# Performance work log

Hardware: AMD Instinct MI355X
Metric: run time of the kernel (lower is better)

## Reference

```python
import jax, jax.numpy as jnp
import numpy as np

# ---- config ----
N = 500000
C = 32            # output_coordinate_dim
RES = [256, 256, 256, 64]
J = 2             # wavelet levels
BOUNDS = 1.3
# plane i -> (H, W) of stored plane, and (q, r) coord indices into [x,y,z,t]
# grid_sample convention: coord0 indexes W, coord1 indexes H
PLANE_RES = [(256, 256), (256, 256), (256, 64), (256, 256), (256, 64), (256, 64)]
COORD_IDX = [(0, 1), (0, 2), (3, 0), (1, 2), (3, 1), (3, 2)]

# coif4 decomposition low-pass filter (pywt), 24 taps
DEC_LO = np.array([
    -1.7849850030882614e-06, -3.2596802368833675e-06, 3.1229875865345646e-05,
    6.233903446100713e-05, -0.00025997455248771324, -0.0005890207562443383,
    0.0012665619292989445, 0.003751436157278457, -0.00565828668661072,
    -0.015211731527946259, 0.025082261844864097, 0.03933442712333749,
    -0.09622044203398798, -0.06662747426342504, 0.4343860564914685,
    0.782238930920499, 0.41530840703043026, -0.05607731331675481,
    -0.08126669968087875, 0.026682300156053072, 0.016068943964776348,
    -0.0073461663276420935, -0.0016294920126017326, 0.0008923136685823146],
    dtype=np.float32)
REC_LO = DEC_LO[::-1].copy()                                    # synthesis low-pass
REC_HI = (DEC_LO * ((-1.0) ** np.arange(DEC_LO.shape[0]))).astype(np.float32)  # QMF high-pass


def _up2(x, axis):
    """Insert zeros between samples along axis (upsample by 2)."""
    x = jnp.moveaxis(x, axis, -1)
    z = jnp.zeros(x.shape[:-1] + (2 * x.shape[-1],), x.dtype)
    z = z.at[..., ::2].set(x)
    return jnp.moveaxis(z, -1, axis)


def _circ_conv(x, f, axis):
    """Circular convolution along axis with a short fixed filter (periodization mode)."""
    out = f[0] * x
    for k in range(1, len(f)):
        out = out + f[k] * jnp.roll(x, k, axis=axis)
    return out


def _sfb1d(lo, hi, axis):
    """1D synthesis filter bank: upsample, filter, add. Length L -> 2L."""
    return _circ_conv(_up2(lo, axis), REC_LO, axis) + _circ_conv(_up2(hi, axis), REC_HI, axis)


def _sfb_level(ll, yh):
    """One inverse-DWT level. ll: [1,C,h,w], yh: [1,C,3,h,w] -> [1,C,2h,2w]."""
    lh, hl, hh = yh[:, :, 0], yh[:, :, 1], yh[:, :, 2]
    lo = _sfb1d(ll, lh, axis=2)   # combine along H
    hi = _sfb1d(hl, hh, axis=2)
    return _sfb1d(lo, hi, axis=3)  # combine along W


def _idwt2(yl, yhb, yha):
    """2-level inverse DWT (coif4, periodization). yl coarsest, yhb coarse detail, yha fine detail."""
    x = _sfb_level(yl, yhb)   # H/4 -> H/2
    x = _sfb_level(x, yha)    # H/2 -> H
    return x                  # [1, C, H, W]


def _bilinear_sample(plane, coords):
    """torch.grid_sample(bilinear, align_corners=True) equivalent.
    plane: [C,H,W]; coords: [N,2] in [-1,1], coords[:,0]->W, coords[:,1]->H. Returns [N,C]."""
    Cc, H, W = plane.shape
    x = jnp.clip((coords[:, 0] + 1.0) * 0.5 * (W - 1), 0.0, W - 1.0)
    y = jnp.clip((coords[:, 1] + 1.0) * 0.5 * (H - 1), 0.0, H - 1.0)
    x0 = jnp.clip(jnp.floor(x), 0.0, W - 2.0)
    y0 = jnp.clip(jnp.floor(y), 0.0, H - 2.0)
    wx = x - x0
    wy = y - y0
    x0i = x0.astype(jnp.int32); x1i = x0i + 1
    y0i = y0.astype(jnp.int32); y1i = y0i + 1
    v = (plane[:, y0i, x0i] * (1 - wy) * (1 - wx)
         + plane[:, y0i, x1i] * (1 - wy) * wx
         + plane[:, y1i, x0i] * wy * (1 - wx)
         + plane[:, y1i, x1i] * wy * wx)  # [C,N]
    return v.T


def setup_inputs() -> dict:
    key = jax.random.key(0)
    keys = jax.random.split(key, 2 + 6 * 3)
    inp = {}
    inp["pts"] = jax.random.uniform(keys[0], (N, 3), jnp.float32, -BOUNDS, BOUNDS)
    inp["timestamps"] = jax.random.uniform(keys[1], (N, 1), jnp.float32, 0.0, 1.0)
    for i, (H, W) in enumerate(PLANE_RES):
        k0, k1, k2 = keys[2 + 3 * i], keys[2 + 3 * i + 1], keys[2 + 3 * i + 2]
        # wavelet-domain learned parameters: yl coarsest approx, yha fine detail, yhb coarse detail
        inp[f"yl{i}"] = 0.3 + 0.1 * jax.random.normal(k0, (1, C, H // 4, W // 4), jnp.float32)
        inp[f"yha{i}"] = 0.05 * jax.random.normal(k1, (1, C, 3, H // 2, W // 2), jnp.float32)
        inp[f"yhb{i}"] = 0.05 * jax.random.normal(k2, (1, C, 3, H // 4, W // 4), jnp.float32)
    return inp


def reference(pts, timestamps,
              yl0, yha0, yhb0, yl1, yha1, yhb1, yl2, yha2, yhb2,
              yl3, yha3, yhb3, yl4, yha4, yhb4, yl5, yha5, yhb5):
    coefs = [(yl0, yha0, yhb0), (yl1, yha1, yhb1), (yl2, yha2, yhb2),
             (yl3, yha3, yhb3), (yl4, yha4, yhb4), (yl5, yha5, yhb5)]
    # normalize_aabb with aabb = [[B,B,B],[-B,-B,-B]]
    pts_n = (pts - BOUNDS) * (2.0 / (-2.0 * BOUNDS)) - 1.0
    t = timestamps * 2.0 - 1.0
    p4 = jnp.concatenate([pts_n, t], axis=-1)  # [N,4] = (x,y,z,t) in [-1,1]
    interp = jnp.ones((), jnp.float32)
    for (yl, yha, yhb), (q, r) in zip(coefs, COORD_IDX):
        plane = _idwt2(yl, yhb, yha)[0]                      # [C,H,W] IDWT reconstruction
        coords = jnp.stack([p4[:, q], p4[:, r]], axis=-1)    # [N,2]
        feat = _bilinear_sample(plane, coords)               # [N,C] gather
        interp = interp * feat                               # multiplicative fusion
    return interp
```

## Files before the change

### kernel.cpp

```cpp
#include <hip/hip_runtime.h>
#include <hip/hip_fp16.h>

#define NBIN 4096
#define NREP 8
#define SCAP 32
#define OVCAP 65536

__device__ __constant__ float DEC_LO[24] = {
    -1.7849850030882614e-06f, -3.2596802368833675e-06f, 3.1229875865345646e-05f,
    6.233903446100713e-05f, -0.00025997455248771324f, -0.0005890207562443383f,
    0.0012665619292989445f, 0.003751436157278457f, -0.00565828668661072f,
    -0.015211731527946259f, 0.025082261844864097f, 0.03933442712333749f,
    -0.09622044203398798f, -0.06662747426342504f, 0.4343860564914685f,
    0.782238930920499f, 0.41530840703043026f, -0.05607731331675481f,
    -0.08126669968087875f, 0.026682300156053072f, 0.016068943964776348f,
    -0.0073461663276420935f, -0.0016294920126017326f, 0.0008923136685823146f
};

struct PK {
    const float* yl[6];
    const float* yhb[6];
    const float* yha[6];
    float* x1[6];
    __half* lo2[6];
    __half* hi2[6];
    __half* planeH[6];
    const float* pts;
    const float* ts;
    int* cnt;
    float4* binP4;
    int* binIdx;
    float4* ovP4;
    int* ovIdx;
    int Npts;
};

__device__ __forceinline__ void compute_p4(const float* pts, const float* ts, int p, float* p4) {
    const float sc = (float)(2.0 / (-2.0 * 1.3));
    p4[0] = (pts[p * 3 + 0] - 1.3f) * sc - 1.0f;
    p4[1] = (pts[p * 3 + 1] - 1.3f) * sc - 1.0f;
    p4[2] = (pts[p * 3 + 2] - 1.3f) * sc - 1.0f;
    p4[3] = ts[p] * 2.0f - 1.0f;
}

__device__ __forceinline__ int morton_key(const float* p4) {
    int key = 0;
#pragma unroll
    for (int d = 0; d < 4; ++d) {
        float u = (p4[d] + 1.0f) * 0.5f * 8.0f;
        int ci = (int)u;
        ci = ci < 0 ? 0 : (ci > 7 ? 7 : ci);
#pragma unroll
        for (int b = 0; b < 3; ++b) key |= ((ci >> b) & 1) << (b * 4 + d);
    }
    return key;
}

__global__ __launch_bounds__(256) void k1_l1_zero(PK a) {
    __shared__ struct { float lo[32 * 64], hi[32 * 64]; } sm;
    int bid = blockIdx.x, tid = threadIdx.x;

    if (bid < 768) {
        int rg = bid & 3, c = (bid >> 2) & 31, i = bid >> 7;
        int w4 = (i == 0 || i == 1 || i == 3) ? 64 : 16;
        int lw4 = (w4 == 64) ? 6 : 4;

        const float* llc = a.yl[i] + (size_t)c * 64 * w4;
        const float* lhc = a.yhb[i] + (size_t)(c * 3 + 0) * 64 * w4;
        const float* hlc = a.yhb[i] + (size_t)(c * 3 + 1) * 64 * w4;
        const float* hhc = a.yhb[i] + (size_t)(c * 3 + 2) * 64 * w4;

        for (int idx = tid; idx < (16 << lw4); idx += 256) {
            int mp = idx >> lw4, x = idx & (w4 - 1);
            int m = rg * 16 + mp;
            float lo0 = 0.f, lo1 = 0.f, hi0 = 0.f, hi1 = 0.f;
#pragma unroll
            for (int j = 0; j < 12; ++j) {
                int r = (m - j) & 63;
                int ii = (r << lw4) + x;
                float vll = llc[ii], vlh = lhc[ii], vhl = hlc[ii], vhh = hhc[ii];
                float rl0 = DEC_LO[23 - 2 * j], rl1 = DEC_LO[22 - 2 * j];
                float rh0 = DEC_LO[2 * j],      rh1 = -DEC_LO[2 * j + 1];
                lo0 += rl0 * vll + rh0 * vlh;
                lo1 += rl1 * vll + rh1 * vlh;
                hi0 += rl0 * vhl + rh0 * vhh;
                hi1 += rl1 * vhl + rh1 * vhh;
            }
            sm.lo[((2 * mp) << lw4) + x] = lo0;
            sm.lo[((2 * mp + 1) << lw4) + x] = lo1;
            sm.hi[((2 * mp) << lw4) + x] = hi0;
            sm.hi[((2 * mp + 1) << lw4) + x] = hi1;
        }
        __syncthreads();

        int w2 = w4 * 2;
        float* x1p = a.x1[i] + (size_t)c * 128 * w2;
        for (int idx = tid; idx < (32 << lw4); idx += 256) {
            int yl = idx >> lw4, mcol = idx & (w4 - 1);
            float o0 = 0.f, o1 = 0.f;
#pragma unroll
            for (int j = 0; j < 12; ++j) {
                int r = (mcol - j) & (w4 - 1);
                float vl = sm.lo[(yl << lw4) + r], vh = sm.hi[(yl << lw4) + r];
                o0 += DEC_LO[23 - 2 * j] * vl + DEC_LO[2 * j] * vh;
                o1 += DEC_LO[22 - 2 * j] * vl - DEC_LO[2 * j + 1] * vh;
            }
            *(float2*)(x1p + (size_t)(rg * 32 + yl) * w2 + 2 * mcol) = make_float2(o0, o1);
        }
    } else {
        int idx = (bid - 768) * 256 + tid;
        if (idx <= NREP * NBIN) a.cnt[idx] = 0;
    }
}

__global__ __launch_bounds__(256) void k2_v2_scatter(PK a) {
    int bid = blockIdx.x, tid = threadIdx.x;

    if (bid < 512) {
        const int S = 512 * 256;
        int rep = bid & 7;
        int t = bid * 256 + tid;
        for (int base = 0; base < a.Npts; base += 4 * S) {
            float4 q[4];
            int key[4], pi[4], pos[4];
#pragma unroll
            for (int k = 0; k < 4; ++k) {
                int p = base + t + k * S;
                pi[k] = p;
                if (p < a.Npts) {
                    float p4[4];
                    compute_p4(a.pts, a.ts, p, p4);
                    key[k] = morton_key(p4);
                    q[k] = make_float4(p4[0], p4[1], p4[2], p4[3]);
                } else {
                    key[k] = -1;
                }
            }
#pragma unroll
            for (int k = 0; k < 4; ++k)
                if (key[k] >= 0) pos[k] = atomicAdd(&a.cnt[rep * NBIN + key[k]], 1);
#pragma unroll
            for (int k = 0; k < 4; ++k) {
                if (key[k] < 0) continue;
                if (pos[k] < SCAP) {
                    size_t slot = ((size_t)rep * NBIN + key[k]) * SCAP + pos[k];
                    a.binP4[slot] = q[k];
                    a.binIdx[slot] = pi[k];
                } else {
                    int ov = atomicAdd(&a.cnt[NREP * NBIN], 1);
                    if (ov < OVCAP) {
                        a.ovP4[ov] = q[k];
                        a.ovIdx[ov] = pi[k];
                    }
                }
            }
        }
    } else {
        int ib = bid - 512;
        ib = (ib & 7) * 240 + (ib >> 3);

        const int boff[7] = {0, 512, 1024, 1152, 1664, 1792, 1920};
        int i = 0;
        while (i < 5 && ib >= boff[i + 1]) ++i;
        int lw2 = (i == 0 || i == 1 || i == 3) ? 7 : 5;
        int w2 = 1 << lw2;
        unsigned t = (unsigned)(ib - boff[i]) * 256u + tid;
        unsigned tpc = 32u << lw2;
        unsigned c = t >> (5 + lw2);
        unsigned rem = t & (tpc - 1);
        unsigned m = rem >> (lw2 - 2);
        unsigned x = (rem & (unsigned)((w2 >> 2) - 1)) * 4;
        unsigned hw = 128u << lw2;

        const float* llc = a.x1[i] + (size_t)c * hw;
        const float* lhc = a.yha[i] + (size_t)(c * 3 + 0) * hw;
        const float* hlc = a.yha[i] + (size_t)(c * 3 + 1) * hw;
        const float* hhc = a.yha[i] + (size_t)(c * 3 + 2) * hw;

        float4 acl0 = {0,0,0,0}, acl1 = {0,0,0,0}, ach0 = {0,0,0,0}, ach1 = {0,0,0,0};
#pragma unroll
        for (int j = 0; j < 12; ++j) {
            int r = ((int)m - j) & 127;
            unsigned idx = ((unsigned)r << lw2) + x;
            float4 vll = *(const float4*)(llc + idx);
            float4 vlh = *(const float4*)(lhc + idx);
            float4 vhl = *(const float4*)(hlc + idx);
            float4 vhh = *(const float4*)(hhc + idx);
            float rl0 = DEC_LO[23 - 2 * j], rl1 = DEC_LO[22 - 2 * j];
            float rh0 = DEC_LO[2 * j],      rh1 = -DEC_LO[2 * j + 1];
            acl0.x += rl0 * vll.x + rh0 * vlh.x;  acl0.y += rl0 * vll.y + rh0 * vlh.y;
            acl0.z += rl0 * vll.z + rh0 * vlh.z;  acl0.w += rl0 * vll.w + rh0 * vlh.w;
            acl1.x += rl1 * vll.x + rh1 * vlh.x;  acl1.y += rl1 * vll.y + rh1 * vlh.y;
            acl1.z += rl1 * vll.z + rh1 * vlh.z;  acl1.w += rl1 * vll.w + rh1 * vlh.w;
            ach0.x += rl0 * vhl.x + rh0 * vhh.x;  ach0.y += rl0 * vhl.y + rh0 * vhh.y;
            ach0.z += rl0 * vhl.z + rh0 * vhh.z;  ach0.w += rl0 * vhl.w + rh0 * vhh.w;
            ach1.x += rl1 * vhl.x + rh1 * vhh.x;  ach1.y += rl1 * vhl.y + rh1 * vhh.y;
            ach1.z += rl1 * vhl.z + rh1 * vhh.z;  ach1.w += rl1 * vhl.w + rh1 * vhh.w;
        }
        size_t ob = ((size_t)c * 256 + 2 * m) * w2 + x;
        __half* lp = a.lo2[i] + ob;
        *(__half2*)(lp)          = __floats2half2_rn(acl0.x, acl0.y);
        *(__half2*)(lp + 2)      = __floats2half2_rn(acl0.z, acl0.w);
        *(__half2*)(lp + w2)     = __floats2half2_rn(acl1.x, acl1.y);
        *(__half2*)(lp + w2 + 2) = __floats2half2_rn(acl1.z, acl1.w);
        __half* hpp = a.hi2[i] + ob;
        *(__half2*)(hpp)          = __floats2half2_rn(ach0.x, ach0.y);
        *(__half2*)(hpp + 2)      = __floats2half2_rn(ach0.z, ach0.w);
        *(__half2*)(hpp + w2)     = __floats2half2_rn(ach1.x, ach1.y);
        *(__half2*)(hpp + w2 + 2) = __floats2half2_rn(ach1.z, ach1.w);
    }
}

__global__ __launch_bounds__(256) void k3_ht(PK a) {
    __shared__ struct { __half lo[32 * 130], hi[32 * 130]; } sm;
    int bid = blockIdx.x, tid = threadIdx.x;
    int i = bid >> 8, y = bid & 255;
    int lw2 = (i == 0 || i == 1 || i == 3) ? 7 : 5;
    int w2 = 1 << lw2;
    int stride = w2 + 2;

    for (int idx = tid; idx < (32 << lw2); idx += 256) {
        int c = idx >> lw2, x = idx & (w2 - 1);
        size_t g = ((size_t)c * 256 + y) * w2 + x;
        sm.lo[c * stride + x] = a.lo2[i][g];
        sm.hi[c * stride + x] = a.hi2[i][g];
    }
    __syncthreads();

    int W = 2 * w2;
    __half* orow = a.planeH[i] + (size_t)y * W * 32;
    for (int idx = tid; idx < (32 << lw2); idx += 256) {
        int m = idx >> 5, c = idx & 31;
        float o0 = 0.f, o1 = 0.f;
#pragma unroll
        for (int j = 0; j < 12; ++j) {
            int r2 = m - j; if (r2 < 0) r2 += w2;
            float vl = __half2float(sm.lo[c * stride + r2]);
            float vh = __half2float(sm.hi[c * stride + r2]);
            o0 += DEC_LO[23 - 2 * j] * vl + DEC_LO[2 * j] * vh;
            o1 += DEC_LO[22 - 2 * j] * vl - DEC_LO[2 * j + 1] * vh;
        }
        orow[(2 * m) * 32 + c] = __float2half(o0);
        orow[(2 * m + 1) * 32 + c] = __float2half(o1);
    }
}

union H8 { float4 f4; __half h[8]; };

struct SK {
    const __half* pl[6];
    const float4* binP4;
    const int* binIdx;
    const int* cnt;
    const float4* ovP4;
    const int* ovIdx;
    float* out;
};

__device__ __forceinline__ void sample_pair(const SK& a,
        const float* p4A, int oA, int chA,
        const float* p4B, int oB, int chB, bool hasB) {
    const int PW[6] = {256, 256, 64, 256, 64, 64};
    const int QI[6] = {0, 0, 3, 1, 3, 3};
    const int RI[6] = {1, 2, 0, 2, 1, 2};
    float accA[8] = {1.f, 1.f, 1.f, 1.f, 1.f, 1.f, 1.f, 1.f};
    float accB[8] = {1.f, 1.f, 1.f, 1.f, 1.f, 1.f, 1.f, 1.f};
#pragma unroll
    for (int i = 0; i < 6; ++i) {
        int W = PW[i];
        float fxA = fminf(fmaxf((p4A[QI[i]] + 1.0f) * 0.5f * (float)(W - 1), 0.0f), (float)(W - 1));
        float fyA = fminf(fmaxf((p4A[RI[i]] + 1.0f) * 0.5f * 255.0f, 0.0f), 255.0f);
        float x0A = fminf(floorf(fxA), (float)(W - 2));
        float y0A = fminf(floorf(fyA), 254.0f);
        float wxA = fxA - x0A, wyA = fyA - y0A;
        const __half* baseA = a.pl[i] + ((size_t)(int)y0A * W + (int)x0A) * 32 + chA;
        float fxB = fminf(fmaxf((p4B[QI[i]] + 1.0f) * 0.5f * (float)(W - 1), 0.0f), (float)(W - 1));
        float fyB = fminf(fmaxf((p4B[RI[i]] + 1.0f) * 0.5f * 255.0f, 0.0f), 255.0f);
        float x0B = fminf(floorf(fxB), (float)(W - 2));
        float y0B = fminf(floorf(fyB), 254.0f);
        float wxB = fxB - x0B, wyB = fyB - y0B;
        const __half* baseB = a.pl[i] + ((size_t)(int)y0B * W + (int)x0B) * 32 + chB;

        H8 a00, a01, a10, a11, b00, b01, b10, b11;
        a00.f4 = *(const float4*)(baseA);
        a01.f4 = *(const float4*)(baseA + 32);
        a10.f4 = *(const float4*)(baseA + (size_t)W * 32);
        a11.f4 = *(const float4*)(baseA + (size_t)W * 32 + 32);
        b00.f4 = *(const float4*)(baseB);
        b01.f4 = *(const float4*)(baseB + 32);
        b10.f4 = *(const float4*)(baseB + (size_t)W * 32);
        b11.f4 = *(const float4*)(baseB + (size_t)W * 32 + 32);

        float wA00 = (1.f - wyA) * (1.f - wxA), wA01 = (1.f - wyA) * wxA;
        float wA10 = wyA * (1.f - wxA), wA11 = wyA * wxA;
        float wB00 = (1.f - wyB) * (1.f - wxB), wB01 = (1.f - wyB) * wxB;
        float wB10 = wyB * (1.f - wxB), wB11 = wyB * wxB;
#pragma unroll
        for (int k = 0; k < 8; ++k) {
            accA[k] *= wA00 * __half2float(a00.h[k]) + wA01 * __half2float(a01.h[k]) +
                       wA10 * __half2float(a10.h[k]) + wA11 * __half2float(a11.h[k]);
            accB[k] *= wB00 * __half2float(b00.h[k]) + wB01 * __half2float(b01.h[k]) +
                       wB10 * __half2float(b10.h[k]) + wB11 * __half2float(b11.h[k]);
        }
    }
    float* opA = a.out + (size_t)oA * 32 + chA;
    *(float4*)(opA)     = make_float4(accA[0], accA[1], accA[2], accA[3]);
    *(float4*)(opA + 4) = make_float4(accA[4], accA[5], accA[6], accA[7]);
    if (hasB) {
        float* opB = a.out + (size_t)oB * 32 + chB;
        *(float4*)(opB)     = make_float4(accB[0], accB[1], accB[2], accB[3]);
        *(float4*)(opB + 4) = make_float4(accB[4], accB[5], accB[6], accB[7]);
    }
}

__global__ __launch_bounds__(256) void k4_sample(SK a) {
    int bid = blockIdx.x, tid = threadIdx.x;
    if (bid < NBIN) {
        int bin = (bid & 7) * (NBIN / 8) + (bid >> 3);

        int pre[NREP + 1];
        pre[0] = 0;
#pragma unroll
        for (int r = 0; r < NREP; ++r) {
            int c = a.cnt[r * NBIN + bin];
            pre[r + 1] = pre[r] + (c < SCAP ? c : SCAP);
        }
        int n4 = pre[NREP] * 4;

        for (int l0 = tid; l0 < n4; l0 += 512) {
            int l1 = l0 + 256;
            bool hasB = l1 < n4;
            int lB = hasB ? l1 : l0;

            int sA = l0 >> 2, chA = (l0 & 3) << 3;
            int sB = lB >> 2, chB = (lB & 3) << 3;
            int rA = 0, rB = 0;
#pragma unroll
            for (int rr = 1; rr < NREP; ++rr) {
                if (sA >= pre[rr]) rA = rr;
                if (sB >= pre[rr]) rB = rr;
            }
            size_t slotA = ((size_t)rA * NBIN + bin) * SCAP + (sA - pre[rA]);
            size_t slotB = ((size_t)rB * NBIN + bin) * SCAP + (sB - pre[rB]);
            float4 qA = a.binP4[slotA];
            float4 qB = a.binP4[slotB];
            int oA = a.binIdx[slotA];
            int oB = a.binIdx[slotB];
            float p4A[4] = {qA.x, qA.y, qA.z, qA.w};
            float p4B[4] = {qB.x, qB.y, qB.z, qB.w};
            sample_pair(a, p4A, oA, chA, p4B, oB, chB, hasB);
        }
    } else {
        int ov = a.cnt[NREP * NBIN];
        ov = ov < OVCAP ? ov : OVCAP;
        int ov4 = ov * 4;
        for (int l0 = (bid - NBIN) * 256 + tid; l0 < ov4; l0 += 4096) {
            int l1 = l0 + 2048;
            bool hasB = l1 < ov4;
            int lB = hasB ? l1 : l0;
            int sA = l0 >> 2, chA = (l0 & 3) << 3;
            int sB = lB >> 2, chB = (lB & 3) << 3;
            float4 qA = a.ovP4[sA];
            float4 qB = a.ovP4[sB];
            float p4A[4] = {qA.x, qA.y, qA.z, qA.w};
            float p4B[4] = {qB.x, qB.y, qB.z, qB.w};
            sample_pair(a, p4A, a.ovIdx[sA], chA, p4B, a.ovIdx[sB], chB, hasB);
        }
    }
}

extern "C" void kernel_launch(void* const* d_in, const int* in_sizes, int n_in,
                              void* d_out, int out_size, void* d_ws, size_t ws_size,
                              hipStream_t stream) {
    const int PWt[6] = {256, 256, 64, 256, 64, 64};
    const int Npts = in_sizes[0] / 3;

    char* ws = (char*)d_ws;
    PK a;
    size_t off = 0;
    for (int i = 0; i < 6; ++i) {
        int W = PWt[i], w2 = W / 2;
        a.x1[i] = (float*)(ws + off);      off += (size_t)32 * 128 * w2 * 4;
        a.lo2[i] = (__half*)(ws + off);    off += (size_t)32 * 256 * w2 * 2;
        a.hi2[i] = (__half*)(ws + off);    off += (size_t)32 * 256 * w2 * 2;
        a.planeH[i] = (__half*)(ws + off); off += (size_t)256 * W * 32 * 2;
    }
    off = (off + 15) & ~(size_t)15;
    a.binP4 = (float4*)(ws + off);  off += (size_t)NREP * NBIN * SCAP * 16;
    a.ovP4 = (float4*)(ws + off);   off += (size_t)OVCAP * 16;
    a.binIdx = (int*)(ws + off);    off += (size_t)NREP * NBIN * SCAP * 4;
    a.ovIdx = (int*)(ws + off);     off += (size_t)OVCAP * 4;
    a.cnt = (int*)(ws + off);       off += ((size_t)NREP * NBIN + 1) * 4;

    a.pts = (const float*)d_in[0];
    a.ts = (const float*)d_in[1];
    for (int i = 0; i < 6; ++i) {
        a.yl[i] = (const float*)d_in[2 + 3 * i];
        a.yha[i] = (const float*)d_in[3 + 3 * i];
        a.yhb[i] = (const float*)d_in[4 + 3 * i];
    }
    a.Npts = Npts;

    k1_l1_zero<<<768 + 129, 256, 0, stream>>>(a);
    k2_v2_scatter<<<512 + 1920, 256, 0, stream>>>(a);
    k3_ht<<<1536, 256, 0, stream>>>(a);

    SK s;
    for (int i = 0; i < 6; ++i) s.pl[i] = a.planeH[i];
    s.binP4 = a.binP4; s.binIdx = a.binIdx; s.cnt = a.cnt;
    s.ovP4 = a.ovP4; s.ovIdx = a.ovIdx;
    s.out = (float*)d_out;
    k4_sample<<<NBIN + 8, 256, 0, stream>>>(s);
}
```

Before: 252.6 us.

## Precompute per-bin prefix counts in k3 and process several bins per sample block

Adds a small extra set of blocks to the transform kernel that computes, for each bin, the capped prefix sums of the per-replica counts and stores them in a new workspace array. The sampling kernel now loads these prefixes with two vector loads instead of eight scattered count loads. Each sampling block handles four consecutive bins, which cuts the block count by four and is meant to reduce launch and per-block overhead for bins holding only a few points. The trade-off is fewer blocks to spread across the GPU and serial bin processing inside a block, which can increase tail imbalance.

```diff
diff --git a/kernel.cpp b/kernel.cpp
--- a/kernel.cpp
+++ b/kernel.cpp
@@ -5,6 +5,7 @@
 #define NREP 8
 #define SCAP 32
 #define OVCAP 65536
+#define BPB 4
 
 __device__ __constant__ float DEC_LO[24] = {
     -1.7849850030882614e-06f, -3.2596802368833675e-06f, 3.1229875865345646e-05f,
@@ -28,6 +29,7 @@
     const float* pts;
     const float* ts;
     int* cnt;
+    int* cum;
     float4* binP4;
     int* binIdx;
     float4* ovP4;
@@ -214,34 +216,46 @@
 __global__ __launch_bounds__(256) void k3_ht(PK a) {
     __shared__ struct { __half lo[32 * 130], hi[32 * 130]; } sm;
     int bid = blockIdx.x, tid = threadIdx.x;
-    int i = bid >> 8, y = bid & 255;
-    int lw2 = (i == 0 || i == 1 || i == 3) ? 7 : 5;
-    int w2 = 1 << lw2;
-    int stride = w2 + 2;
-
-    for (int idx = tid; idx < (32 << lw2); idx += 256) {
-        int c = idx >> lw2, x = idx & (w2 - 1);
-        size_t g = ((size_t)c * 256 + y) * w2 + x;
-        sm.lo[c * stride + x] = a.lo2[i][g];
-        sm.hi[c * stride + x] = a.hi2[i][g];
-    }
-    __syncthreads();
-
-    int W = 2 * w2;
-    __half* orow = a.planeH[i] + (size_t)y * W * 32;
-    for (int idx = tid; idx < (32 << lw2); idx += 256) {
-        int m = idx >> 5, c = idx & 31;
-        float o0 = 0.f, o1 = 0.f;
-#pragma unroll
-        for (int j = 0; j < 12; ++j) {
-            int r2 = m - j; if (r2 < 0) r2 += w2;
-            float vl = __half2float(sm.lo[c * stride + r2]);
-            float vh = __half2float(sm.hi[c * stride + r2]);
-            o0 += DEC_LO[23 - 2 * j] * vl + DEC_LO[2 * j] * vh;
-            o1 += DEC_LO[22 - 2 * j] * vl - DEC_LO[2 * j + 1] * vh;
-        }
-        orow[(2 * m) * 32 + c] = __float2half(o0);
-        orow[(2 * m + 1) * 32 + c] = __float2half(o1);
+
+    if (bid < 1536) {
+        int i = bid >> 8, y = bid & 255;
+        int lw2 = (i == 0 || i == 1 || i == 3) ? 7 : 5;
+        int w2 = 1 << lw2;
+        int stride = w2 + 2;
+
+        for (int idx = tid; idx < (32 << lw2); idx += 256) {
+            int c = idx >> lw2, x = idx & (w2 - 1);
+            size_t g = ((size_t)c * 256 + y) * w2 + x;
+            sm.lo[c * stride + x] = a.lo2[i][g];
+            sm.hi[c * stride + x] = a.hi2[i][g];
+        }
+        __syncthreads();
+
+        int W = 2 * w2;
+        __half* orow = a.planeH[i] + (size_t)y * W * 32;
+        for (int idx = tid; idx < (32 << lw2); idx += 256) {
+            int m = idx >> 5, c = idx & 31;
+            float o0 = 0.f, o1 = 0.f;
+#pragma unroll
+            for (int j = 0; j < 12; ++j) {
+                int r2 = m - j; if (r2 < 0) r2 += w2;
+                float vl = __half2float(sm.lo[c * stride + r2]);
+                float vh = __half2float(sm.hi[c * stride + r2]);
+                o0 += DEC_LO[23 - 2 * j] * vl + DEC_LO[2 * j] * vh;
+                o1 += DEC_LO[22 - 2 * j] * vl - DEC_LO[2 * j + 1] * vh;
+            }
+            orow[(2 * m) * 32 + c] = __float2half(o0);
+            orow[(2 * m + 1) * 32 + c] = __float2half(o1);
+        }
+    } else {
+        int bin = (bid - 1536) * 256 + tid;
+        int c = 0;
+#pragma unroll
+        for (int r = 0; r < NREP; ++r) {
+            int v = a.cnt[r * NBIN + bin];
+            c += (v < SCAP ? v : SCAP);
+            a.cum[bin * 8 + r] = c;
+        }
     }
 }
 
@@ -252,6 +266,7 @@
     const float4* binP4;
     const int* binIdx;
     const int* cnt;
+    const int* cum;
     const float4* ovP4;
     const int* ovIdx;
     float* out;
@@ -315,46 +330,47 @@
 
 __global__ __launch_bounds__(256) void k4_sample(SK a) {
     int bid = blockIdx.x, tid = threadIdx.x;
-    if (bid < NBIN) {
-        int bin = (bid & 7) * (NBIN / 8) + (bid >> 3);
-
-        int pre[NREP + 1];
-        pre[0] = 0;
-#pragma unroll
-        for (int r = 0; r < NREP; ++r) {
-            int c = a.cnt[r * NBIN + bin];
-            pre[r + 1] = pre[r] + (c < SCAP ? c : SCAP);
-        }
-        int n4 = pre[NREP] * 4;
-
-        for (int l0 = tid; l0 < n4; l0 += 512) {
-            int l1 = l0 + 256;
-            bool hasB = l1 < n4;
-            int lB = hasB ? l1 : l0;
-
-            int sA = l0 >> 2, chA = (l0 & 3) << 3;
-            int sB = lB >> 2, chB = (lB & 3) << 3;
-            int rA = 0, rB = 0;
-#pragma unroll
-            for (int rr = 1; rr < NREP; ++rr) {
-                if (sA >= pre[rr]) rA = rr;
-                if (sB >= pre[rr]) rB = rr;
-            }
-            size_t slotA = ((size_t)rA * NBIN + bin) * SCAP + (sA - pre[rA]);
-            size_t slotB = ((size_t)rB * NBIN + bin) * SCAP + (sB - pre[rB]);
-            float4 qA = a.binP4[slotA];
-            float4 qB = a.binP4[slotB];
-            int oA = a.binIdx[slotA];
-            int oB = a.binIdx[slotB];
-            float p4A[4] = {qA.x, qA.y, qA.z, qA.w};
-            float p4B[4] = {qB.x, qB.y, qB.z, qB.w};
-            sample_pair(a, p4A, oA, chA, p4B, oB, chB, hasB);
+    if (bid < NBIN / BPB) {
+        int xcd = bid & 7, g = bid >> 3;
+        int binBase = xcd * (NBIN / 8) + g * BPB;
+
+#pragma unroll
+        for (int bb = 0; bb < BPB; ++bb) {
+            int bin = binBase + bb;
+            int4 u0 = *(const int4*)(a.cum + bin * 8);
+            int4 u1 = *(const int4*)(a.cum + bin * 8 + 4);
+            int cums[8] = {u0.x, u0.y, u0.z, u0.w, u1.x, u1.y, u1.z, u1.w};
+            int n4 = cums[7] * 4;
+
+            for (int l0 = tid; l0 < n4; l0 += 512) {
+                int l1 = l0 + 256;
+                bool hasB = l1 < n4;
+                int lB = hasB ? l1 : l0;
+
+                int sA = l0 >> 2, chA = (l0 & 3) << 3;
+                int sB = lB >> 2, chB = (lB & 3) << 3;
+                int rA = 0, bsA = 0, rB = 0, bsB = 0;
+#pragma unroll
+                for (int rr = 0; rr < NREP - 1; ++rr) {
+                    if (sA >= cums[rr]) { rA = rr + 1; bsA = cums[rr]; }
+                    if (sB >= cums[rr]) { rB = rr + 1; bsB = cums[rr]; }
+                }
+                size_t slotA = ((size_t)rA * NBIN + bin) * SCAP + (sA - bsA);
+                size_t slotB = ((size_t)rB * NBIN + bin) * SCAP + (sB - bsB);
+                float4 qA = a.binP4[slotA];
+                float4 qB = a.binP4[slotB];
+                int oA = a.binIdx[slotA];
+                int oB = a.binIdx[slotB];
+                float p4A[4] = {qA.x, qA.y, qA.z, qA.w};
+                float p4B[4] = {qB.x, qB.y, qB.z, qB.w};
+                sample_pair(a, p4A, oA, chA, p4B, oB, chB, hasB);
+            }
         }
     } else {
         int ov = a.cnt[NREP * NBIN];
         ov = ov < OVCAP ? ov : OVCAP;
         int ov4 = ov * 4;
-        for (int l0 = (bid - NBIN) * 256 + tid; l0 < ov4; l0 += 4096) {
+        for (int l0 = (bid - NBIN / BPB) * 256 + tid; l0 < ov4; l0 += 4096) {
             int l1 = l0 + 2048;
             bool hasB = l1 < ov4;
             int lB = hasB ? l1 : l0;
@@ -391,6 +407,8 @@
     a.binIdx = (int*)(ws + off);    off += (size_t)NREP * NBIN * SCAP * 4;
     a.ovIdx = (int*)(ws + off);     off += (size_t)OVCAP * 4;
     a.cnt = (int*)(ws + off);       off += ((size_t)NREP * NBIN + 1) * 4;
+    off = (off + 15) & ~(size_t)15;
+    a.cum = (int*)(ws + off);       off += (size_t)NBIN * 8 * 4;
 
     a.pts = (const float*)d_in[0];
     a.ts = (const float*)d_in[1];
@@ -403,12 +421,12 @@
 
     k1_l1_zero<<<768 + 129, 256, 0, stream>>>(a);
     k2_v2_scatter<<<512 + 1920, 256, 0, stream>>>(a);
-    k3_ht<<<1536, 256, 0, stream>>>(a);
+    k3_ht<<<1536 + 16, 256, 0, stream>>>(a);
 
     SK s;
     for (int i = 0; i < 6; ++i) s.pl[i] = a.planeH[i];
-    s.binP4 = a.binP4; s.binIdx = a.binIdx; s.cnt = a.cnt;
+    s.binP4 = a.binP4; s.binIdx = a.binIdx; s.cnt = a.cnt; s.cum = a.cum;
     s.ovP4 = a.ovP4; s.ovIdx = a.ovIdx;
     s.out = (float*)d_out;
-    k4_sample<<<NBIN + 8, 256, 0, stream>>>(s);
-}
+    k4_sample<<<NBIN / BPB + 8, 256, 0, stream>>>(s);
+}
```

New measurement: 249.7 us. About the same (-1.1%).
